# Kernel optimization log

Hardware: AMD Instinct MI355X
Metric: run time of the kernel (lower is better)

## Reference

```python
import jax, jax.numpy as jnp
import numpy as np

B, S, H = 4, 2048, 2048


def _rotate_half(x):
    x1, x2 = jnp.split(x, 2, axis=-1)
    return jnp.concatenate((-x2, x1), axis=-1)


def _rope_tables(seq_len, dim, dtype):
    # standard RoPE over the full hidden dim (emb last dim == dim so it
    # broadcasts against [B,S,dim] activations)
    inv_freq = 1.0 / (10000.0 ** (jnp.arange(0, dim, 2, dtype=jnp.float32) / dim))
    t = jnp.arange(seq_len, dtype=jnp.float32)
    freqs = jnp.einsum('s,d->sd', t, inv_freq)          # [S, dim/2]
    emb = jnp.concatenate((freqs, freqs), axis=-1)      # [S, dim]
    return jnp.cos(emb).astype(dtype)[None], jnp.sin(emb).astype(dtype)[None]  # [1,S,dim]


def setup_inputs() -> dict:
    key = jax.random.key(0)
    ks = jax.random.split(key, 11)
    sc = 0.02
    return {
        'query': jax.random.normal(ks[0], (B, S, H), jnp.float32),
        'key':   jax.random.normal(ks[1], (B, S, H), jnp.float32),
        'value': jax.random.normal(ks[2], (B, S, H), jnp.float32),
        'Wq': jax.random.normal(ks[3], (H, H), jnp.float32) * sc,
        'bq': jax.random.normal(ks[4], (H,), jnp.float32) * sc,
        'Wk': jax.random.normal(ks[5], (H, H), jnp.float32) * sc,
        'bk': jax.random.normal(ks[6], (H,), jnp.float32) * sc,
        'Wv': jax.random.normal(ks[7], (H, H), jnp.float32) * sc,
        'bv': jax.random.normal(ks[8], (H,), jnp.float32) * sc,
        'Wo': jax.random.normal(ks[9], (H, H), jnp.float32) * sc,
        'bo': jax.random.normal(ks[10], (H,), jnp.float32) * sc,
    }


def reference(query, key, value, Wq, bq, Wk, bk, Wv, bv, Wo, bo):
    seq, dim = query.shape[1], query.shape[2]
    cos, sin = _rope_tables(seq, dim, query.dtype)      # [1,S,H]
    q_rot = query * cos + _rotate_half(query) * sin     # RoPE BEFORE projections
    k_rot = key * cos + _rotate_half(key) * sin
    q = jnp.einsum('bsh,oh->bso', q_rot, Wq) + bq       # torch Linear: x @ W.T + b
    k = jnp.einsum('bsh,oh->bso', k_rot, Wk) + bk
    v = jnp.einsum('bsh,oh->bso', value, Wv) + bv
    scale = 1.0 / jnp.sqrt(jnp.asarray(dim, q.dtype))
    scores = jnp.einsum('bqh,bkh->bqk', q, k) * scale   # [B,Sq,Sk]
    probs = jax.nn.softmax(scores, axis=-1)
    context = jnp.einsum('bqk,bkh->bqh', probs, v)
    return jnp.einsum('bsh,oh->bso', context, Wo) + bo
```

## Files before the change

kernel.cpp:

```cpp
#include <hip/hip_runtime.h>


typedef __bf16 bf16_t;
typedef bf16_t bf16x8 __attribute__((ext_vector_type(8)));
typedef bf16_t bf16x4 __attribute__((ext_vector_type(4)));
typedef float  f32x4  __attribute__((ext_vector_type(4)));

#define BDIM 4
#define SDIM 2048
#define HDIM 2048

__device__ __forceinline__ void async_copy16(const bf16_t* g, bf16_t* l) {
  __builtin_amdgcn_global_load_lds(
      (__attribute__((address_space(1))) const void*)g,
      (__attribute__((address_space(3))) void*)l,
      16, 0, 0);
}

__global__ __launch_bounds__(256) void prep_kernel(
    const float* __restrict__ q, const float* __restrict__ k,
    const float* __restrict__ v,
    bf16_t* __restrict__ qr, bf16_t* __restrict__ kr, bf16_t* __restrict__ vb) {
  const int i = blockIdx.x * 256 + threadIdx.x;
  const int j = i & 1023;
  const int row = i >> 10;
  const int s = row & (SDIM - 1);
  const float invf = exp2f(-(float)j * 0.012976281620653759f);
  const float f = (float)s * invf;
  float sn, cs;
  sincosf(f, &sn, &cs);
  const long base = (long)row * HDIM;
  const float q1 = q[base + j], q2 = q[base + j + 1024];
  const float k1 = k[base + j], k2 = k[base + j + 1024];
  qr[base + j]        = (bf16_t)(q1 * cs - q2 * sn);
  qr[base + j + 1024] = (bf16_t)(q2 * cs + q1 * sn);
  kr[base + j]        = (bf16_t)(k1 * cs - k2 * sn);
  kr[base + j + 1024] = (bf16_t)(k2 * cs + k1 * sn);
  vb[base + j]        = (bf16_t)v[base + j];
  vb[base + j + 1024] = (bf16_t)v[base + j + 1024];
}

__global__ __launch_bounds__(256) void wcast_kernel(
    const float* __restrict__ w0, const float* __restrict__ w1,
    const float* __restrict__ w2, const float* __restrict__ w3,
    bf16_t* __restrict__ dst) {
  const int wsel = blockIdx.y;
  const float* src = wsel == 0 ? w0 : wsel == 1 ? w1 : wsel == 2 ? w2 : w3;
  const long i = (long)(blockIdx.x * 256 + threadIdx.x) * 8;
  const float4 a = *(const float4*)&src[i];
  const float4 b = *(const float4*)&src[i + 4];
  bf16x8 o;
  o[0] = (bf16_t)a.x; o[1] = (bf16_t)a.y; o[2] = (bf16_t)a.z; o[3] = (bf16_t)a.w;
  o[4] = (bf16_t)b.x; o[5] = (bf16_t)b.y; o[6] = (bf16_t)b.z; o[7] = (bf16_t)b.w;
  *(bf16x8*)&dst[(long)wsel * HDIM * HDIM + i] = o;
}

template <int OMODE>
__global__ __launch_bounds__(256, 2) void gemm_bt(
    const bf16_t* __restrict__ A, const bf16_t* __restrict__ Bt,
    void* __restrict__ Cv, const float* __restrict__ bias,
    int M, int N, int K, float alpha,
    long sA, long sB, long sC) {
  __shared__ __align__(16) bf16_t As[128 * 64];
  __shared__ __align__(16) bf16_t Bs[128 * 64];
  const int z = blockIdx.z;
  A  += (long)z * sA;
  Bt += (long)z * sB;
  const int tid  = threadIdx.x;
  const int lane = tid & 63;
  const int wave = tid >> 6;
  const int wm = (wave >> 1) * 64;
  const int wn = (wave & 1) * 64;
  const int m0 = blockIdx.y * 128;
  const int n0 = blockIdx.x * 128;
  const int lrow = lane & 15;
  const int quad = lane >> 4;
  const int swz  = lrow & 7;

  f32x4 acc[4][4] = {};

  const long aBase = (long)m0 * K;
  const long bBase = (long)n0 * K;

  const int rl  = lane >> 3;
  const int ccs = ((lane & 7) ^ rl) * 8;

  for (int k0 = 0; k0 < K; k0 += 64) {
#pragma unroll
    for (int i = 0; i < 4; ++i) {
      const int c = wave * 4 + i;
      const int r = c * 8 + rl;
      async_copy16(A  + aBase + (long)r * K + k0 + ccs, As + c * 512);
      async_copy16(Bt + bBase + (long)r * K + k0 + ccs, Bs + c * 512);
    }
    __syncthreads();
#pragma unroll
    for (int ks = 0; ks < 64; ks += 32) {
      bf16x8 af[4], bfr[4];
      const int cg = (ks >> 3) + quad;
      const int j  = (cg ^ swz) * 8;
#pragma unroll
      for (int t = 0; t < 4; ++t)
        af[t] = *(const bf16x8*)&As[(wm + t * 16 + lrow) * 64 + j];
#pragma unroll
      for (int t = 0; t < 4; ++t)
        bfr[t] = *(const bf16x8*)&Bs[(wn + t * 16 + lrow) * 64 + j];
#pragma unroll
      for (int mt = 0; mt < 4; ++mt)
#pragma unroll
        for (int nt = 0; nt < 4; ++nt)
          acc[mt][nt] = __builtin_amdgcn_mfma_f32_16x16x32_bf16(
              af[mt], bfr[nt], acc[mt][nt], 0, 0, 0);
    }
    __syncthreads();
  }

#pragma unroll
  for (int mt = 0; mt < 4; ++mt) {
#pragma unroll
    for (int nt = 0; nt < 4; ++nt) {
      const int col = n0 + wn + nt * 16 + lrow;
      const float bv = bias ? bias[col] : 0.0f;
      if (OMODE == 2) {
        const int row0 = m0 + wm + mt * 16 + quad * 4;
        const int b = row0 >> 11;
        const int s = row0 & (SDIM - 1);
        bf16x4 o;
#pragma unroll
        for (int r = 0; r < 4; ++r) o[r] = (bf16_t)(acc[mt][nt][r] + bv);
        *(bf16x4*)&((bf16_t*)Cv)[(long)b * SDIM * HDIM + (long)col * SDIM + s] = o;
      } else {
#pragma unroll
        for (int r = 0; r < 4; ++r) {
          const int row = m0 + wm + mt * 16 + quad * 4 + r;
          const float v = acc[mt][nt][r] * alpha + bv;
          if (OMODE == 1)
            ((float*)Cv)[(long)z * sC + (long)row * N + col] = v;
          else
            ((bf16_t*)Cv)[(long)z * sC + (long)row * N + col] = (bf16_t)v;
        }
      }
    }
  }
}

__global__ __launch_bounds__(256) void softmax_kernel(
    const bf16_t* __restrict__ Sc, bf16_t* __restrict__ P) {
  const long row = blockIdx.x;
  const bf16_t* src = Sc + row * SDIM;
  bf16_t* dst = P + row * SDIM;
  const int tid = threadIdx.x;
  const bf16x8 in = *(const bf16x8*)&src[tid * 8];
  float x[8];
#pragma unroll
  for (int t = 0; t < 8; ++t) x[t] = (float)in[t];
  float m = x[0];
#pragma unroll
  for (int t = 1; t < 8; ++t) m = fmaxf(m, x[t]);
#pragma unroll
  for (int off = 32; off; off >>= 1) m = fmaxf(m, __shfl_xor(m, off));
  __shared__ float redm[4], reds[4];
  const int wave = tid >> 6, lane = tid & 63;
  if (lane == 0) redm[wave] = m;
  __syncthreads();
  m = fmaxf(fmaxf(redm[0], redm[1]), fmaxf(redm[2], redm[3]));
  float s = 0.0f;
#pragma unroll
  for (int t = 0; t < 8; ++t) { x[t] = __expf(x[t] - m); s += x[t]; }
#pragma unroll
  for (int off = 32; off; off >>= 1) s += __shfl_xor(s, off);
  if (lane == 0) reds[wave] = s;
  __syncthreads();
  s = reds[0] + reds[1] + reds[2] + reds[3];
  const float inv = 1.0f / s;
  bf16x8 o;
#pragma unroll
  for (int t = 0; t < 8; ++t) o[t] = (bf16_t)(x[t] * inv);
  *(bf16x8*)&dst[tid * 8] = o;
}

extern "C" void kernel_launch(void* const* d_in, const int* in_sizes, int n_in,
                              void* d_out, int out_size, void* d_ws, size_t ws_size,
                              hipStream_t stream) {
  const float* q_in = (const float*)d_in[0];
  const float* k_in = (const float*)d_in[1];
  const float* v_in = (const float*)d_in[2];
  const float* Wq = (const float*)d_in[3];
  const float* bq = (const float*)d_in[4];
  const float* Wk = (const float*)d_in[5];
  const float* bk = (const float*)d_in[6];
  const float* Wv = (const float*)d_in[7];
  const float* bv = (const float*)d_in[8];
  const float* Wo = (const float*)d_in[9];
  const float* bo = (const float*)d_in[10];
  float* out = (float*)d_out;

  const size_t ELE  = (size_t)BDIM * SDIM * HDIM;
  const size_t WELE = (size_t)HDIM * HDIM;
  const size_t SEG  = ELE * 2;

  uint8_t* w = (uint8_t*)d_ws;
  bf16_t* qr  = (bf16_t*)(w + 0 * SEG);
  bf16_t* kr  = (bf16_t*)(w + 1 * SEG);
  bf16_t* vb  = (bf16_t*)(w + 2 * SEG);
  bf16_t* Wb  = (bf16_t*)(w + 3 * SEG);
  bf16_t* qp  = (bf16_t*)(w + 4 * SEG);
  bf16_t* kp  = (bf16_t*)(w + 5 * SEG);
  bf16_t* vpT = (bf16_t*)(w + 6 * SEG);
  bf16_t* scores = (bf16_t*)(w + 0 * SEG);
  bf16_t* probs  = (bf16_t*)(w + 2 * SEG);
  bf16_t* ctx    = (bf16_t*)(w + 1 * SEG);

  bf16_t* Wqb = Wb + 0 * WELE;
  bf16_t* Wkb = Wb + 1 * WELE;
  bf16_t* Wvb = Wb + 2 * WELE;
  bf16_t* Wob = Wb + 3 * WELE;

  const dim3 blk(256);
  const long SH = (long)SDIM * HDIM;
  const long SS = (long)SDIM * SDIM;

  prep_kernel<<<dim3(ELE / 2 / 256), blk, 0, stream>>>(q_in, k_in, v_in, qr, kr, vb);
  wcast_kernel<<<dim3(WELE / 8 / 256, 4), blk, 0, stream>>>(Wq, Wk, Wv, Wo, Wb);
  gemm_bt<0><<<dim3(16, 64, 1), blk, 0, stream>>>(qr, Wqb, qp, bq,
      BDIM * SDIM, HDIM, HDIM, 1.0f, 0, 0, 0);
  gemm_bt<0><<<dim3(16, 64, 1), blk, 0, stream>>>(kr, Wkb, kp, bk,
      BDIM * SDIM, HDIM, HDIM, 1.0f, 0, 0, 0);
  gemm_bt<2><<<dim3(16, 64, 1), blk, 0, stream>>>(vb, Wvb, vpT, bv,
      BDIM * SDIM, HDIM, HDIM, 1.0f, 0, 0, 0);
  gemm_bt<0><<<dim3(16, 16, BDIM), blk, 0, stream>>>(qp, kp, scores, nullptr,
      SDIM, SDIM, HDIM, 0.022097086912079612f, SH, SH, SS);
  softmax_kernel<<<dim3(BDIM * SDIM), blk, 0, stream>>>(scores, probs);
  gemm_bt<0><<<dim3(16, 16, BDIM), blk, 0, stream>>>(probs, vpT, ctx, nullptr,
      SDIM, HDIM, SDIM, 1.0f, SS, SH, SH);
  gemm_bt<1><<<dim3(16, 64, 1), blk, 0, stream>>>(ctx, Wob, out, bo,
      BDIM * SDIM, HDIM, HDIM, 1.0f, 0, 0, 0);
}
```

Baseline: 706.7 us.

## Rewrite GEMM as 256x256 tile, 8-wave double-buffered pipelined kernel

Replaces the 128x128, 4-wave GEMM that loads one K-slice and syncs twice per step with a 256x256-tile, 512-thread kernel. It double-buffers 64-wide K slices in 128KB of LDS and interleaves async global->LDS loads of the next quarter-tiles with MFMA quadrants, using explicit vmcnt waits, barriers and setprio. The intent is to hide memory latency behind MFMA work and raise arithmetic intensity per byte loaded. The cost is higher LDS and register use per block, which likely allows only one block per CU despite launch_bounds(512,2), and a fragile hand-written wait schedule. The prefetch wraps with & (K-1), so K must be a power of two.

```diff
diff --git a/kernel.cpp b/kernel.cpp
--- a/kernel.cpp
+++ b/kernel.cpp
@@ -55,68 +55,137 @@
   *(bf16x8*)&dst[(long)wsel * HDIM * HDIM + i] = o;
 }
 
+__device__ __forceinline__ void stage_A_unit(const bf16_t* __restrict__ G, int K,
+                                             int kq, bf16_t* L, int half,
+                                             int wave, int rl, int ccs) {
+#pragma unroll
+  for (int c = 0; c < 2; ++c) {
+    const int idx = c * 8 + wave;
+    const int g = (idx >> 3) * 16 + (idx & 7) + half * 8;
+    async_copy16(G + (long)(g * 8 + rl) * K + kq + ccs, L + g * 512);
+  }
+}
+__device__ __forceinline__ void stage_B_unit(const bf16_t* __restrict__ G, int K,
+                                             int kq, bf16_t* L, int half,
+                                             int wave, int rl, int ccs) {
+#pragma unroll
+  for (int c = 0; c < 2; ++c) {
+    const int idx = c * 8 + wave;
+    const int g = (idx >> 2) * 8 + (idx & 3) + half * 4;
+    async_copy16(G + (long)(g * 8 + rl) * K + kq + ccs, L + g * 512);
+  }
+}
+
 template <int OMODE>
-__global__ __launch_bounds__(256, 2) void gemm_bt(
+__global__ __launch_bounds__(512, 2) void gemm_bt(
     const bf16_t* __restrict__ A, const bf16_t* __restrict__ Bt,
     void* __restrict__ Cv, const float* __restrict__ bias,
     int M, int N, int K, float alpha,
     long sA, long sB, long sC) {
-  __shared__ __align__(16) bf16_t As[128 * 64];
-  __shared__ __align__(16) bf16_t Bs[128 * 64];
+  __shared__ __align__(16) bf16_t lds[4 * 16384];
+  bf16_t* As0 = lds;
+  bf16_t* Bs0 = lds + 16384;
+  bf16_t* As1 = lds + 32768;
+  bf16_t* Bs1 = lds + 49152;
   const int z = blockIdx.z;
   A  += (long)z * sA;
   Bt += (long)z * sB;
   const int tid  = threadIdx.x;
   const int lane = tid & 63;
   const int wave = tid >> 6;
-  const int wm = (wave >> 1) * 64;
-  const int wn = (wave & 1) * 64;
-  const int m0 = blockIdx.y * 128;
-  const int n0 = blockIdx.x * 128;
+  const int wm = (wave >> 2) * 128;
+  const int wn = (wave & 3) * 64;
+  const int m0 = blockIdx.y * 256;
+  const int n0 = blockIdx.x * 256;
   const int lrow = lane & 15;
   const int quad = lane >> 4;
-  const int swz  = lrow & 7;
-
-  f32x4 acc[4][4] = {};
-
-  const long aBase = (long)m0 * K;
-  const long bBase = (long)n0 * K;
-
   const int rl  = lane >> 3;
   const int ccs = ((lane & 7) ^ rl) * 8;
 
-  for (int k0 = 0; k0 < K; k0 += 64) {
-#pragma unroll
-    for (int i = 0; i < 4; ++i) {
-      const int c = wave * 4 + i;
-      const int r = c * 8 + rl;
-      async_copy16(A  + aBase + (long)r * K + k0 + ccs, As + c * 512);
-      async_copy16(Bt + bBase + (long)r * K + k0 + ccs, Bs + c * 512);
-    }
-    __syncthreads();
-#pragma unroll
-    for (int ks = 0; ks < 64; ks += 32) {
-      bf16x8 af[4], bfr[4];
-      const int cg = (ks >> 3) + quad;
-      const int j  = (cg ^ swz) * 8;
-#pragma unroll
-      for (int t = 0; t < 4; ++t)
-        af[t] = *(const bf16x8*)&As[(wm + t * 16 + lrow) * 64 + j];
-#pragma unroll
-      for (int t = 0; t < 4; ++t)
-        bfr[t] = *(const bf16x8*)&Bs[(wn + t * 16 + lrow) * 64 + j];
-#pragma unroll
-      for (int mt = 0; mt < 4; ++mt)
-#pragma unroll
-        for (int nt = 0; nt < 4; ++nt)
-          acc[mt][nt] = __builtin_amdgcn_mfma_f32_16x16x32_bf16(
-              af[mt], bfr[nt], acc[mt][nt], 0, 0, 0);
-    }
-    __syncthreads();
-  }
-
-#pragma unroll
-  for (int mt = 0; mt < 4; ++mt) {
+  const bf16_t* Ab = A  + (long)m0 * K;
+  const bf16_t* Bb = Bt + (long)n0 * K;
+
+  f32x4 acc[8][4] = {};
+
+#define DS_A(AS, MH)                                                         \
+  _Pragma("unroll") for (int ks = 0; ks < 2; ++ks) {                         \
+    const int cg = ks * 4 + quad;                                            \
+    _Pragma("unroll") for (int t = 0; t < 4; ++t) {                          \
+      const int r = wm + ((MH) * 4 + t) * 16 + lrow;                         \
+      af[t][ks] = *(const bf16x8*)&(AS)[r * 64 + ((cg ^ (r & 7)) * 8)];      \
+    }                                                                        \
+  }
+#define DS_B(BS, NH)                                                         \
+  _Pragma("unroll") for (int ks = 0; ks < 2; ++ks) {                         \
+    const int cg = ks * 4 + quad;                                            \
+    _Pragma("unroll") for (int u = 0; u < 2; ++u) {                          \
+      const int r = wn + ((NH) * 2 + u) * 16 + lrow;                         \
+      bfr[u][ks] = *(const bf16x8*)&(BS)[r * 64 + ((cg ^ (r & 7)) * 8)];     \
+    }                                                                        \
+  }
+#define MFMA_Q(MH, NH)                                                       \
+  __builtin_amdgcn_s_barrier();                                              \
+  asm volatile("s_waitcnt lgkmcnt(0)" ::: "memory");                         \
+  __builtin_amdgcn_s_setprio(1);                                             \
+  _Pragma("unroll") for (int ks = 0; ks < 2; ++ks)                           \
+    _Pragma("unroll") for (int t = 0; t < 4; ++t)                            \
+      _Pragma("unroll") for (int u = 0; u < 2; ++u)                          \
+        acc[(MH) * 4 + t][(NH) * 2 + u] =                                    \
+            __builtin_amdgcn_mfma_f32_16x16x32_bf16(                         \
+                af[t][ks], bfr[u][ks], acc[(MH) * 4 + t][(NH) * 2 + u],      \
+                0, 0, 0);                                                    \
+  __builtin_amdgcn_s_setprio(0);
+#define VM_WAIT4 asm volatile("s_waitcnt vmcnt(4)" ::: "memory");
+#define ENDBAR   __builtin_amdgcn_s_barrier();
+
+  stage_A_unit(Ab, K, 0,  As0, 0, wave, rl, ccs);
+  stage_A_unit(Ab, K, 0,  As0, 1, wave, rl, ccs);
+  stage_B_unit(Bb, K, 0,  Bs0, 0, wave, rl, ccs);
+  stage_B_unit(Bb, K, 0,  Bs0, 1, wave, rl, ccs);
+  stage_A_unit(Ab, K, 64, As1, 0, wave, rl, ccs);
+  stage_B_unit(Bb, K, 64, Bs1, 0, wave, rl, ccs);
+  asm volatile("s_waitcnt vmcnt(4)" ::: "memory");
+  __builtin_amdgcn_s_barrier();
+
+  const int Km = K - 1;
+  for (int k0 = 0; k0 < K; k0 += 128) {
+    bf16x8 af[4][2], bfr[2][2];
+    const int kA = k0 + 64;
+    const int kB = (k0 + 128) & Km;
+    const int kC = (k0 + 192) & Km;
+    DS_A(As0, 0) DS_B(Bs0, 0)
+    stage_A_unit(Ab, K, kA, As1, 1, wave, rl, ccs);
+    MFMA_Q(0, 0) ENDBAR
+    DS_B(Bs0, 1)
+    stage_B_unit(Bb, K, kA, Bs1, 1, wave, rl, ccs);
+    MFMA_Q(0, 1) ENDBAR
+    DS_A(As0, 1) DS_B(Bs0, 0)
+    stage_A_unit(Ab, K, kB, As0, 0, wave, rl, ccs);
+    MFMA_Q(1, 0) ENDBAR
+    DS_B(Bs0, 1)
+    stage_B_unit(Bb, K, kB, Bs0, 0, wave, rl, ccs);
+    MFMA_Q(1, 1) VM_WAIT4 ENDBAR
+    DS_A(As1, 0) DS_B(Bs1, 0)
+    stage_A_unit(Ab, K, kB, As0, 1, wave, rl, ccs);
+    MFMA_Q(0, 0) ENDBAR
+    DS_B(Bs1, 1)
+    stage_B_unit(Bb, K, kB, Bs0, 1, wave, rl, ccs);
+    MFMA_Q(0, 1) ENDBAR
+    DS_A(As1, 1) DS_B(Bs1, 0)
+    stage_A_unit(Ab, K, kC, As1, 0, wave, rl, ccs);
+    MFMA_Q(1, 0) ENDBAR
+    DS_B(Bs1, 1)
+    stage_B_unit(Bb, K, kC, Bs1, 0, wave, rl, ccs);
+    MFMA_Q(1, 1) VM_WAIT4 ENDBAR
+  }
+#undef DS_A
+#undef DS_B
+#undef MFMA_Q
+#undef VM_WAIT4
+#undef ENDBAR
+
+#pragma unroll
+  for (int mt = 0; mt < 8; ++mt) {
 #pragma unroll
     for (int nt = 0; nt < 4; ++nt) {
       const int col = n0 + wn + nt * 16 + lrow;
@@ -217,22 +286,23 @@
   bf16_t* Wob = Wb + 3 * WELE;
 
   const dim3 blk(256);
+  const dim3 gblk(512);
   const long SH = (long)SDIM * HDIM;
   const long SS = (long)SDIM * SDIM;
 
   prep_kernel<<<dim3(ELE / 2 / 256), blk, 0, stream>>>(q_in, k_in, v_in, qr, kr, vb);
   wcast_kernel<<<dim3(WELE / 8 / 256, 4), blk, 0, stream>>>(Wq, Wk, Wv, Wo, Wb);
-  gemm_bt<0><<<dim3(16, 64, 1), blk, 0, stream>>>(qr, Wqb, qp, bq,
+  gemm_bt<0><<<dim3(8, 32, 1), gblk, 0, stream>>>(qr, Wqb, qp, bq,
       BDIM * SDIM, HDIM, HDIM, 1.0f, 0, 0, 0);
-  gemm_bt<0><<<dim3(16, 64, 1), blk, 0, stream>>>(kr, Wkb, kp, bk,
+  gemm_bt<0><<<dim3(8, 32, 1), gblk, 0, stream>>>(kr, Wkb, kp, bk,
       BDIM * SDIM, HDIM, HDIM, 1.0f, 0, 0, 0);
-  gemm_bt<2><<<dim3(16, 64, 1), blk, 0, stream>>>(vb, Wvb, vpT, bv,
+  gemm_bt<2><<<dim3(8, 32, 1), gblk, 0, stream>>>(vb, Wvb, vpT, bv,
       BDIM * SDIM, HDIM, HDIM, 1.0f, 0, 0, 0);
-  gemm_bt<0><<<dim3(16, 16, BDIM), blk, 0, stream>>>(qp, kp, scores, nullptr,
+  gemm_bt<0><<<dim3(8, 8, BDIM), gblk, 0, stream>>>(qp, kp, scores, nullptr,
       SDIM, SDIM, HDIM, 0.022097086912079612f, SH, SH, SS);
   softmax_kernel<<<dim3(BDIM * SDIM), blk, 0, stream>>>(scores, probs);
-  gemm_bt<0><<<dim3(16, 16, BDIM), blk, 0, stream>>>(probs, vpT, ctx, nullptr,
+  gemm_bt<0><<<dim3(8, 8, BDIM), gblk, 0, stream>>>(probs, vpT, ctx, nullptr,
       SDIM, HDIM, SDIM, 1.0f, SS, SH, SH);
-  gemm_bt<1><<<dim3(16, 64, 1), blk, 0, stream>>>(ctx, Wob, out, bo,
+  gemm_bt<1><<<dim3(8, 32, 1), gblk, 0, stream>>>(ctx, Wob, out, bo,
       BDIM * SDIM, HDIM, HDIM, 1.0f, 0, 0, 0);
 }
```

Measured after the change: 653.7 us. -7.5%, faster.
